# Performance work log

Hardware: AMD Instinct MI355X
Metric: run time of the kernel (lower is better)

## Reference

```python
import jax, jax.numpy as jnp
import numpy as np

VOCAB = 32000
NUM_STATE = 256
NLABEL = 64
BATCH = 128
MAXLEN = 256
# transition init scale chosen so E[e^2]*S*a^2/3 ~= 1 -> per-step magnitude ~constant
TRANS_A = 0.208


def setup_inputs() -> dict:
    key = jax.random.key(0)
    k1, k2, k3, k4 = jax.random.split(key, 4)
    sentences = jax.random.randint(k1, (BATCH, MAXLEN), 0, VOCAB, dtype=jnp.int64)
    # original init: input.weight ~ U(0.5, 0.5) (constant 0.5). Use U(0.25, 0.75) so the
    # emission stays bounded away from 0 (it is divided by) while not being degenerate.
    emb = jax.random.uniform(k2, (VOCAB, NUM_STATE), minval=0.25, maxval=0.75, dtype=jnp.float32)
    transition = jax.random.uniform(k3, (NUM_STATE, NUM_STATE), minval=-TRANS_A, maxval=TRANS_A, dtype=jnp.float32)
    output = jax.random.uniform(k4, (NUM_STATE, NLABEL), minval=-0.5, maxval=0.5, dtype=jnp.float32)
    return {"sentences": sentences, "emb": emb, "transition": transition, "output": output}


def reference(sentences, emb, transition, output):
    # emission: [maxlen, batch, num_state]
    em = emb[sentences.T]

    def step_fwd(carry, e):  # carry: [B,S]
        nxt = jnp.einsum('ij,bj->bi', transition, carry) * e
        return nxt, nxt

    _, fw_rest = jax.lax.scan(step_fwd, em[0], em[1:])
    forwards = jnp.concatenate([em[:1], fw_rest], axis=0)  # [L,B,S]

    em_rev = em[::-1]

    def step_bwd(carry, e):  # uses transition^T
        nxt = jnp.einsum('ji,bj->bi', transition, carry) * e
        return nxt, nxt

    _, bw_rest = jax.lax.scan(step_bwd, em_rev[0], em_rev[1:])
    backwards = jnp.concatenate([em_rev[:1], bw_rest], axis=0)[::-1]  # time-aligned [L,B,S]

    expected_count = forwards * backwards / em
    score = jnp.einsum('lbs,sn->lbn', expected_count, output)
    return score.transpose(1, 0, 2)  # [batch, maxlen, nlabel]
```

## Files before the change

kernel.cpp:

```cpp
#include <hip/hip_runtime.h>
#include <hip/hip_bf16.h>


typedef _Float16 half8 __attribute__((ext_vector_type(8)));
typedef _Float16 half4 __attribute__((ext_vector_type(4)));
typedef float    f32x4 __attribute__((ext_vector_type(4)));
typedef unsigned long long u64;

#define LL 256
#define BB 128
#define SS 256
#define BT 16
#define RSTR8 67
#define RSTRO 65

static __device__ __forceinline__ f32x4 mfma16f(half8 a, half8 b, f32x4 c) {
  return __builtin_amdgcn_mfma_f32_16x16x32_f16(a, b, c, 0, 0, 0);
}

static __device__ __forceinline__ void lds_barrier() {
  __asm__ __volatile__("s_waitcnt lgkmcnt(0)\n\ts_barrier" ::: "memory");
}

static __device__ __forceinline__ u64 pack4(f32x4 v) {
  union { half4 h; u64 u; } x;
  x.h[0] = (_Float16)v[0];
  x.h[1] = (_Float16)v[1];
  x.h[2] = (_Float16)v[2];
  x.h[3] = (_Float16)v[3];
  return x.u;
}

static __device__ __forceinline__ half8 read_frag_s(const u64* plane, int row,
                                                    int kt, int q, int stride8) {
  const int o = row * stride8 + kt * 8 + q * 2;
  union { u64 u[2]; half8 v; } x;
  x.u[0] = plane[o];
  x.u[1] = plane[o + 1];
  return x.v;
}

__global__ __launch_bounds__(512, 2)
void hmm_chain(const int* __restrict__ sent, const float* __restrict__ emb,
               const float* __restrict__ T, _Float16* __restrict__ fwh,
               _Float16* __restrict__ gh)
{
  __shared__ u64 s_carry[2][BT * RSTR8];
  __shared__ int s_tok[BT * 257];

  const int tid  = threadIdx.x;
  const int lane = tid & 63;
  const int w    = tid >> 6;
  const int m    = lane & 15;
  const int q    = lane >> 4;

  const int  bid = blockIdx.x;
  const bool fwd = (bid < 8);
  const int  bg0 = (fwd ? bid : bid - 8) * BT;
  _Float16* const obuf = fwd ? fwh : gh;

  for (int idx = tid; idx < BT * LL; idx += 512) {
    int bb = idx >> 8, l2 = idx & 255;
    s_tok[bb * 257 + l2] = sent[(bg0 + bb) * LL + l2];
  }
  __syncthreads();

  half8 a_h[2][8];
#pragma unroll
  for (int mt = 0; mt < 2; ++mt) {
#pragma unroll
    for (int kt = 0; kt < 8; ++kt) {
      const int r0 = 32 * w + 16 * mt + m;
      const int kb = 32 * kt + 8 * q;
      float v[8];
      if (fwd) {
        f32x4 f0 = *(const f32x4*)(T + r0 * 256 + kb);
        f32x4 f1 = *(const f32x4*)(T + r0 * 256 + kb + 4);
#pragma unroll
        for (int j = 0; j < 4; ++j) { v[j] = f0[j]; v[4 + j] = f1[j]; }
      } else {
#pragma unroll
        for (int j = 0; j < 8; ++j) v[j] = T[(kb + j) * 256 + r0];
      }
      half8 hi;
#pragma unroll
      for (int j = 0; j < 8; ++j) hi[j] = (_Float16)v[j];
      a_h[mt][kt] = hi;
    }
  }

  const int l0 = fwd ? 0 : (LL - 1);
  {
    const int tok0 = s_tok[m * 257 + l0];
#pragma unroll
    for (int mt = 0; mt < 2; ++mt) {
      const int st = 32 * w + 16 * mt + 4 * q;
      f32x4 e0 = *(const f32x4*)(emb + (size_t)tok0 * 256 + st);
      u64 pc = pack4(e0);
      f32x4 one = 1.0f;
      u64 po = fwd ? pc : pack4(one);
      *(u64*)(obuf + (size_t)(l0 * BB + bg0 + m) * SS + st) = po;
      s_carry[0][m * RSTR8 + 8 * w + 4 * mt + q] = pc;
    }
  }

  f32x4 em_q0[2], em_q1[2];
  {
    const int la = fwd ? 1 : (LL - 2);
    const int lb = fwd ? 2 : (LL - 3);
    const int ta = s_tok[m * 257 + la];
    const int tb = s_tok[m * 257 + lb];
#pragma unroll
    for (int mt = 0; mt < 2; ++mt) {
      em_q0[mt] = *(const f32x4*)(emb + (size_t)ta * 256 + 32 * w + 16 * mt + 4 * q);
      em_q1[mt] = *(const f32x4*)(emb + (size_t)tb * 256 + 32 * w + 16 * mt + 4 * q);
    }
  }
  __syncthreads();

  for (int s = 1; s < LL; ++s) {
    const int l  = fwd ? s : (LL - 1) - s;
    const int rb = (s - 1) & 1, wb = s & 1;

    const u64* pr = &s_carry[rb][0];
    half8 bfr[8];
#pragma unroll
    for (int kt = 0; kt < 8; ++kt)
      bfr[kt] = read_frag_s(pr, m, kt, q, RSTR8);

    f32x4 em_now[2];
#pragma unroll
    for (int mt = 0; mt < 2; ++mt) { em_now[mt] = em_q0[mt]; em_q0[mt] = em_q1[mt]; }
    {
      const int ln = fwd ? (s + 2 < LL ? s + 2 : LL - 1)
                         : ((LL - 3) - s > 0 ? (LL - 3) - s : 0);
      const int tokn = s_tok[m * 257 + ln];
#pragma unroll
      for (int mt = 0; mt < 2; ++mt)
        em_q1[mt] = *(const f32x4*)(emb + (size_t)tokn * 256 + 32 * w + 16 * mt + 4 * q);
    }

    f32x4 hh0 = 0.0f, hh1 = 0.0f;
#pragma unroll
    for (int kt = 0; kt < 8; ++kt) {
      hh0 = mfma16f(a_h[0][kt], bfr[kt], hh0);
      hh1 = mfma16f(a_h[1][kt], bfr[kt], hh1);
    }
    f32x4 v[2] = { hh0, hh1 };

#pragma unroll
    for (int mt = 0; mt < 2; ++mt) {
      const int st = 32 * w + 16 * mt + 4 * q;
      f32x4 cn = v[mt] * em_now[mt];
      u64 p0 = pack4(cn);
      s_carry[wb][m * RSTR8 + 8 * w + 4 * mt + q] = p0;
      u64 sv = fwd ? p0 : pack4(v[mt]);
      *(u64*)(obuf + (size_t)(l * BB + bg0 + m) * SS + st) = sv;
    }
    lds_barrier();
  }
}

__global__ __launch_bounds__(256, 2)
void hmm_score(const _Float16* __restrict__ fwh, const _Float16* __restrict__ gh,
               const float* __restrict__ outm, float* __restrict__ score)
{
  __shared__ u64 p_pl[64 * RSTR8];
  __shared__ u64 o_pl[64 * RSTRO];

  const int tid  = threadIdx.x;
  const int lane = tid & 63;
  const int w    = tid >> 6;
  const int rh   = w >> 1;
  const int np   = w & 1;
  const int m    = lane & 15;
  const int q    = lane >> 4;
  const int R0   = blockIdx.x * 64;

  {
    _Float16* o_h = (_Float16*)o_pl;
    for (int i = tid; i < 4096; i += 256) {
      f32x4 v = *(const f32x4*)(outm + i * 4);
      int k = i >> 4, n0 = (i & 15) * 4;
#pragma unroll
      for (int r = 0; r < 4; ++r)
        o_h[(n0 + r) * (RSTRO * 4) + k] = (_Float16)v[r];
    }
  }

  for (int idx = tid; idx < 64 * 64; idx += 256) {
    int row = idx >> 6, c = idx & 63;
    union { u64 u; half4 h; } a, b, p;
    a.u = *(const u64*)(fwh + (size_t)(R0 + row) * 256 + c * 4);
    b.u = *(const u64*)(gh  + (size_t)(R0 + row) * 256 + c * 4);
    p.h = a.h * b.h;
    p_pl[row * RSTR8 + c] = p.u;
  }
  lds_barrier();

  f32x4 acc[2][2];
#pragma unroll
  for (int j = 0; j < 2; ++j)
#pragma unroll
    for (int jn = 0; jn < 2; ++jn) acc[j][jn] = 0.0f;

#pragma unroll
  for (int kt = 0; kt < 8; ++kt) {
    half8 of[2];
#pragma unroll
    for (int jn = 0; jn < 2; ++jn)
      of[jn] = read_frag_s(o_pl, 16 * (2 * np + jn) + m, kt, q, RSTRO);
#pragma unroll
    for (int j = 0; j < 2; ++j) {
      half8 pf = read_frag_s(p_pl, 32 * rh + 16 * j + m, kt, q, RSTR8);
#pragma unroll
      for (int jn = 0; jn < 2; ++jn)
        acc[j][jn] = mfma16f(pf, of[jn], acc[j][jn]);
    }
  }

#pragma unroll
  for (int j = 0; j < 2; ++j) {
#pragma unroll
    for (int jn = 0; jn < 2; ++jn) {
#pragma unroll
      for (int r = 0; r < 4; ++r) {
        int row = R0 + 32 * rh + 16 * j + 4 * q + r;
        int l = row >> 7, b = row & 127;
        score[(size_t)b * 16384 + l * 64 + 16 * (2 * np + jn) + m] = acc[j][jn][r];
      }
    }
  }
}

extern "C" void kernel_launch(void* const* d_in, const int* in_sizes, int n_in,
                              void* d_out, int out_size, void* d_ws, size_t ws_size,
                              hipStream_t stream) {
  (void)in_sizes; (void)n_in; (void)out_size; (void)ws_size;
  const int*   sent = (const int*)d_in[0];
  const float* emb  = (const float*)d_in[1];
  const float* T    = (const float*)d_in[2];
  const float* outm = (const float*)d_in[3];
  _Float16* fwh = (_Float16*)d_ws;
  _Float16* gh  = fwh + (size_t)LL * BB * SS;

  hmm_chain<<<16, 512, 0, stream>>>(sent, emb, T, fwh, gh);
  hmm_score<<<512, 256, 0, stream>>>(fwh, gh, outm, (float*)d_out);
}
```

Before: 296.1 us.

## Replace per-step block barrier with per-wave LDS flags in recurrence chain

```diff
diff --git a/kernel.cpp b/kernel.cpp
--- a/kernel.cpp
+++ b/kernel.cpp
@@ -20,6 +20,10 @@
 
 static __device__ __forceinline__ void lds_barrier() {
   __asm__ __volatile__("s_waitcnt lgkmcnt(0)\n\ts_barrier" ::: "memory");
+}
+
+static __device__ __forceinline__ void lds_drain() {
+  __asm__ __volatile__("s_waitcnt lgkmcnt(0)" ::: "memory");
 }
 
 static __device__ __forceinline__ u64 pack4(f32x4 v) {
@@ -47,6 +51,7 @@
 {
   __shared__ u64 s_carry[2][BT * RSTR8];
   __shared__ int s_tok[BT * 257];
+  __shared__ int s_flag[8];
 
   const int tid  = threadIdx.x;
   const int lane = tid & 63;
@@ -58,6 +63,9 @@
   const bool fwd = (bid < 8);
   const int  bg0 = (fwd ? bid : bid - 8) * BT;
   _Float16* const obuf = fwd ? fwh : gh;
+  volatile int* vflag = s_flag;
+
+  if (tid < 8) s_flag[tid] = -1;
 
   for (int idx = tid; idx < BT * LL; idx += 512) {
     int bb = idx >> 8, l2 = idx & 255;
@@ -69,7 +77,8 @@
 #pragma unroll
   for (int mt = 0; mt < 2; ++mt) {
 #pragma unroll
-    for (int kt = 0; kt < 8; ++kt) {
+    for (int j = 0; j < 8; ++j) {
+      const int kt = (w + j) & 7;
       const int r0 = 32 * w + 16 * mt + m;
       const int kb = 32 * kt + 8 * q;
       float v[8];
@@ -77,15 +86,15 @@
         f32x4 f0 = *(const f32x4*)(T + r0 * 256 + kb);
         f32x4 f1 = *(const f32x4*)(T + r0 * 256 + kb + 4);
 #pragma unroll
-        for (int j = 0; j < 4; ++j) { v[j] = f0[j]; v[4 + j] = f1[j]; }
+        for (int jj = 0; jj < 4; ++jj) { v[jj] = f0[jj]; v[4 + jj] = f1[jj]; }
       } else {
 #pragma unroll
-        for (int j = 0; j < 8; ++j) v[j] = T[(kb + j) * 256 + r0];
+        for (int jj = 0; jj < 8; ++jj) v[jj] = T[(kb + jj) * 256 + r0];
       }
       half8 hi;
 #pragma unroll
-      for (int j = 0; j < 8; ++j) hi[j] = (_Float16)v[j];
-      a_h[mt][kt] = hi;
+      for (int jj = 0; jj < 8; ++jj) hi[jj] = (_Float16)v[jj];
+      a_h[mt][j] = hi;
     }
   }
 
@@ -103,6 +112,8 @@
       s_carry[0][m * RSTR8 + 8 * w + 4 * mt + q] = pc;
     }
   }
+  lds_drain();
+  if (lane == 0) vflag[w] = 0;
 
   f32x4 em_q0[2], em_q1[2];
   {
@@ -116,21 +127,51 @@
       em_q1[mt] = *(const f32x4*)(emb + (size_t)tb * 256 + 32 * w + 16 * mt + 4 * q);
     }
   }
-  __syncthreads();
 
   for (int s = 1; s < LL; ++s) {
-    const int l  = fwd ? s : (LL - 1) - s;
-    const int rb = (s - 1) & 1, wb = s & 1;
+    const int l    = fwd ? s : (LL - 1) - s;
+    const int rb   = (s - 1) & 1, wb = s & 1;
+    const int need = s - 1;
 
     const u64* pr = &s_carry[rb][0];
-    half8 bfr[8];
-#pragma unroll
-    for (int kt = 0; kt < 8; ++kt)
-      bfr[kt] = read_frag_s(pr, m, kt, q, RSTR8);
+
+    f32x4 hh0 = 0.0f, hh1 = 0.0f;
+    int fl_pre = 0;
+#pragma unroll
+    for (int j = 0; j < 8; ++j) {
+      const int u = (w + j) & 7;
+      if (j > 0) {
+        int fl = fl_pre;
+        while (fl < need) fl = vflag[u];
+      }
+      if (j < 7) fl_pre = vflag[(w + j + 1) & 7];
+      __asm__ __volatile__("" ::: "memory");
+      half8 bfr = read_frag_s(pr, m, u, q, RSTR8);
+      hh0 = mfma16f(a_h[0][j], bfr, hh0);
+      hh1 = mfma16f(a_h[1][j], bfr, hh1);
+    }
+    f32x4 v[2] = { hh0, hh1 };
 
     f32x4 em_now[2];
 #pragma unroll
     for (int mt = 0; mt < 2; ++mt) { em_now[mt] = em_q0[mt]; em_q0[mt] = em_q1[mt]; }
+
+    u64 sv[2];
+#pragma unroll
+    for (int mt = 0; mt < 2; ++mt) {
+      f32x4 cn = v[mt] * em_now[mt];
+      u64 p0 = pack4(cn);
+      s_carry[wb][m * RSTR8 + 8 * w + 4 * mt + q] = p0;
+      sv[mt] = fwd ? p0 : pack4(v[mt]);
+    }
+    lds_drain();
+    if (lane == 0) vflag[w] = s;
+
+#pragma unroll
+    for (int mt = 0; mt < 2; ++mt) {
+      const int st = 32 * w + 16 * mt + 4 * q;
+      *(u64*)(obuf + (size_t)(l * BB + bg0 + m) * SS + st) = sv[mt];
+    }
     {
       const int ln = fwd ? (s + 2 < LL ? s + 2 : LL - 1)
                          : ((LL - 3) - s > 0 ? (LL - 3) - s : 0);
@@ -139,25 +180,6 @@
       for (int mt = 0; mt < 2; ++mt)
         em_q1[mt] = *(const f32x4*)(emb + (size_t)tokn * 256 + 32 * w + 16 * mt + 4 * q);
     }
-
-    f32x4 hh0 = 0.0f, hh1 = 0.0f;
-#pragma unroll
-    for (int kt = 0; kt < 8; ++kt) {
-      hh0 = mfma16f(a_h[0][kt], bfr[kt], hh0);
-      hh1 = mfma16f(a_h[1][kt], bfr[kt], hh1);
-    }
-    f32x4 v[2] = { hh0, hh1 };
-
-#pragma unroll
-    for (int mt = 0; mt < 2; ++mt) {
-      const int st = 32 * w + 16 * mt + 4 * q;
-      f32x4 cn = v[mt] * em_now[mt];
-      u64 p0 = pack4(cn);
-      s_carry[wb][m * RSTR8 + 8 * w + 4 * mt + q] = p0;
-      u64 sv = fwd ? p0 : pack4(v[mt]);
-      *(u64*)(obuf + (size_t)(l * BB + bg0 + m) * SS + st) = sv;
-    }
-    lds_barrier();
   }
 }
 
```

After: 401.0 us. +35.4%, slower.
